# Kernel tuning notes

Hardware: AMD Instinct MI355X
Metric: run time of the kernel (lower is better)

The kernel has to match this reference:

```python
import jax, jax.numpy as jnp
import numpy as np

EPS = 1e-8
ACT_BITS = 8


def _ternary_vq(t):
    gamma = jnp.abs(t).mean()
    q = jnp.clip(jnp.round(t / (gamma + EPS)), -1.0, 1.0)
    return q * gamma


def setup_inputs() -> dict:
    key = jax.random.key(0)
    k1, k2, k3 = jax.random.split(key, 3)
    in_features, out_features = 1024, 1024
    x = jax.random.normal(k1, (8, 4096, in_features), dtype=jnp.float32)
    weight = jax.random.normal(k2, (out_features, in_features), dtype=jnp.float32)
    bias = jax.random.normal(k3, (out_features,), dtype=jnp.float32)
    return {"x": x, "weight": weight, "bias": bias}


def reference(x, weight, bias):
    # Weight/bias ternary quantization (done once in __init__ of the module)
    wq = _ternary_vq(weight)   # [out, in]
    bq = _ternary_vq(bias)     # [out]

    # Activation quantization: power-of-two scale from global absmax
    qmax = jnp.float32(2 ** (ACT_BITS - 1) - 1)  # 127
    max_val = jnp.max(jnp.abs(x))
    scale = jnp.exp2(jnp.floor(jnp.log2(max_val / qmax + EPS)))
    xq = jnp.round(jnp.clip(x, -qmax * scale, qmax * scale) / scale) * scale

    # F.linear: x @ W^T + b
    return jnp.einsum('bsi,oi->bso', xq, wq) + bq
```

## Files before the change

### kernel.cpp

```cpp
#include <hip/hip_runtime.h>

typedef __attribute__((ext_vector_type(4))) int int4v;

constexpr int Mdim = 32768;
constexpr int Kdim = 1024;
constexpr int Ndim = 1024;
constexpr float FEPS = 1e-8f;

constexpr size_t WQ_OFF = 32768;
constexpr size_t XQ_OFF = WQ_OFF + (size_t)Ndim * Kdim;
constexpr size_t WS_NEED = XQ_OFF + (size_t)Mdim * Kdim;

__device__ __forceinline__ void gload16(const void* g, void* l) {
  __builtin_amdgcn_global_load_lds(
      (const __attribute__((address_space(1))) unsigned int*)g,
      (__attribute__((address_space(3))) unsigned int*)l, 16, 0, 0);
}

__global__ void k_absmax(const uint4* __restrict__ xv, unsigned* __restrict__ pmax, int n4) {
  int i0 = blockIdx.x * blockDim.x + threadIdx.x;
  int stride = gridDim.x * blockDim.x;
  unsigned m = 0u;
  for (int i = i0; i < n4; i += stride) {
    uint4 v = xv[i];
    m = max(m, v.x & 0x7fffffffu);
    m = max(m, v.y & 0x7fffffffu);
    m = max(m, v.z & 0x7fffffffu);
    m = max(m, v.w & 0x7fffffffu);
  }
  #pragma unroll
  for (int off = 32; off > 0; off >>= 1)
    m = max(m, (unsigned)__shfl_down((int)m, off, 64));
  __shared__ unsigned red[4];
  if ((threadIdx.x & 63) == 0) red[threadIdx.x >> 6] = m;
  __syncthreads();
  if (threadIdx.x == 0) {
    unsigned r = max(max(red[0], red[1]), max(red[2], red[3]));
    pmax[blockIdx.x] = r;
  }
}

__global__ void k_wsum(const float4* __restrict__ wv, float* __restrict__ partials, int n4) {
  float s = 0.f;
  int stride = gridDim.x * blockDim.x;
  for (int i = blockIdx.x * blockDim.x + threadIdx.x; i < n4; i += stride) {
    float4 v = wv[i];
    s += fabsf(v.x) + fabsf(v.y) + fabsf(v.z) + fabsf(v.w);
  }
  __shared__ float red[256];
  red[threadIdx.x] = s;
  __syncthreads();
  for (int h = 128; h > 0; h >>= 1) {
    if (threadIdx.x < h) red[threadIdx.x] += red[threadIdx.x + h];
    __syncthreads();
  }
  if (threadIdx.x == 0) partials[blockIdx.x] = red[0];
}

__global__ void k_finalize(const float* __restrict__ bias, const float* __restrict__ partials,
                           const unsigned* __restrict__ pmax,
                           float* __restrict__ scalars, float* __restrict__ bq) {
  __shared__ float redf[256];
  __shared__ unsigned redu[256];
  __shared__ float sh_gb;
  int t = threadIdx.x;

  float s = fabsf(bias[t]) + fabsf(bias[t + 256]) + fabsf(bias[t + 512]) + fabsf(bias[t + 768]);
  redf[t] = s;
  unsigned m = 0u;
  #pragma unroll
  for (int i = 0; i < 8; ++i) m = max(m, pmax[t + 256 * i]);
  redu[t] = m;
  __syncthreads();
  for (int h = 128; h > 0; h >>= 1) {
    if (t < h) {
      redf[t] += redf[t + h];
      redu[t] = max(redu[t], redu[t + h]);
    }
    __syncthreads();
  }
  if (t == 0) {
    float gb = redf[0] / 1024.0f;
    float sw = 0.f;
    for (int i = 0; i < 256; ++i) sw += partials[i];
    float gw = sw / (1024.0f * 1024.0f);
    float maxval = __uint_as_float(redu[0]);
    float v = maxval / 127.0f + FEPS;
    int e = (int)((__float_as_uint(v) >> 23) & 0xff) - 127;
    float scale = ldexpf(1.0f, e);
    scalars[0] = gw;
    scalars[1] = gb;
    scalars[2] = scale;
    scalars[3] = scale * gw;
    scalars[4] = 127.0f * scale;
    scalars[5] = ldexpf(1.0f, -e);
    sh_gb = gb;
  }
  __syncthreads();
  float gb = sh_gb;
  for (int i = t; i < 1024; i += 256) {
    float q = rintf(bias[i] / (gb + FEPS));
    q = fminf(fmaxf(q, -1.0f), 1.0f);
    bq[i] = q * gb;
  }
}

__device__ __forceinline__ int qact8(float v, float qs, float inv) {
  return (int)rintf(fminf(fmaxf(v, -qs), qs) * inv);
}

__global__ void k_wquant(const float* __restrict__ w, const float* __restrict__ scalars,
                         unsigned char* __restrict__ wq) {
  float inv_g = scalars[0] + FEPS;
  int wave = (blockIdx.x * blockDim.x + threadIdx.x) >> 6;
  int lane = threadIdx.x & 63;
  int nb = wave >> 4;
  int kt = wave & 15;
  int r = lane >> 2;
  int c = lane & 3;
  const float4* src = (const float4*)(w + (size_t)(nb * 16 + r) * Kdim + kt * 64 + c * 16);
  unsigned o[4];
  #pragma unroll
  for (int v = 0; v < 4; ++v) {
    float4 f = src[v];
    int a = (int)rintf(fminf(fmaxf(f.x / inv_g, -1.f), 1.f));
    int b = (int)rintf(fminf(fmaxf(f.y / inv_g, -1.f), 1.f));
    int cc = (int)rintf(fminf(fmaxf(f.z / inv_g, -1.f), 1.f));
    int d = (int)rintf(fminf(fmaxf(f.w / inv_g, -1.f), 1.f));
    o[v] = (unsigned)(a & 0xff) | ((unsigned)(b & 0xff) << 8) |
           ((unsigned)(cc & 0xff) << 16) | ((unsigned)(d & 0xff) << 24);
  }
  uint4 pk; pk.x = o[0]; pk.y = o[1]; pk.z = o[2]; pk.w = o[3];
  *(uint4*)(wq + (size_t)wave * 1024 + c * 256 + r * 16) = pk;
}

__global__ void k_xquant(const float* __restrict__ x, const float* __restrict__ scalars,
                         unsigned char* __restrict__ xq) {
  float qs = scalars[4], inv = scalars[5];
  int wave = (blockIdx.x * blockDim.x + threadIdx.x) >> 6;
  int lane = threadIdx.x & 63;
  int mb = wave >> 4;
  int kt = wave & 15;
  int r = lane >> 2;
  int c = lane & 3;
  const float4* src = (const float4*)(x + (size_t)(mb * 16 + r) * Kdim + kt * 64 + c * 16);
  unsigned o[4];
  #pragma unroll
  for (int v = 0; v < 4; ++v) {
    float4 f = src[v];
    o[v] = (unsigned)(qact8(f.x, qs, inv) & 0xff) |
           ((unsigned)(qact8(f.y, qs, inv) & 0xff) << 8) |
           ((unsigned)(qact8(f.z, qs, inv) & 0xff) << 16) |
           ((unsigned)(qact8(f.w, qs, inv) & 0xff) << 24);
  }
  uint4 pk; pk.x = o[0]; pk.y = o[1]; pk.z = o[2]; pk.w = o[3];
  *(uint4*)(xq + (size_t)wave * 1024 + c * 256 + r * 16) = pk;
}

__launch_bounds__(256)
__global__ void k_gemm(const unsigned char* __restrict__ xq, const unsigned char* __restrict__ wq,
                       const float* __restrict__ scalars, const float* __restrict__ bq,
                       float* __restrict__ out) {
  __shared__ __align__(16) unsigned char lds[3 * 16384];

  const int tid = threadIdx.x;
  const int lane = tid & 63;
  const int wv = tid >> 6;
  const int wr = wv >> 1;
  const int wc = wv & 1;

  int bid = blockIdx.x;
  int swz = (bid & 7) * ((int)gridDim.x >> 3) + (bid >> 3);
  const int mtile = swz >> 3;
  const int ntile = swz & 7;
  const int m0 = mtile * 128;
  const int n0 = ntile * 128;

  const unsigned char* gA0 = xq + ((size_t)(mtile * 8 + wv) * 16) * 1024 + lane * 16;
  const unsigned char* gA1 = xq + ((size_t)(mtile * 8 + wv + 4) * 16) * 1024 + lane * 16;
  const unsigned char* gB0 = wq + ((size_t)(ntile * 8 + wv) * 16) * 1024 + lane * 16;
  const unsigned char* gB1 = wq + ((size_t)(ntile * 8 + wv + 4) * 16) * 1024 + lane * 16;
  const int lA0 = wv * 1024, lA1 = (wv + 4) * 1024;
  const int lB0 = 8192 + wv * 1024, lB1 = 8192 + (wv + 4) * 1024;

#define STAGE(kt, buf) do {                                   \
    unsigned char* base_ = lds + (buf) * 16384;               \
    gload16(gA0 + (size_t)(kt) * 1024, base_ + lA0);          \
    gload16(gA1 + (size_t)(kt) * 1024, base_ + lA1);          \
    gload16(gB0 + (size_t)(kt) * 1024, base_ + lB0);          \
    gload16(gB1 + (size_t)(kt) * 1024, base_ + lB1);          \
  } while (0)

  int4v acc[4][4];
  #pragma unroll
  for (int i = 0; i < 4; ++i)
    #pragma unroll
    for (int j = 0; j < 4; ++j)
      acc[i][j] = (int4v){0, 0, 0, 0};

  const int aoff = wr * 4 * 1024 + lane * 16;
  const int boff = 8192 + wc * 4 * 1024 + lane * 16;

  STAGE(0, 0);
  STAGE(1, 1);

  int cur = 0;
  for (int kt = 0; kt < 15; ++kt) {
    asm volatile("s_waitcnt vmcnt(4)" ::: "memory");
    __builtin_amdgcn_s_barrier();
    asm volatile("" ::: "memory");
    const unsigned char* bufp = lds + cur * 16384;
    int4v a[4], b[4];
    #pragma unroll
    for (int mi = 0; mi < 4; ++mi)
      a[mi] = *(const int4v*)(bufp + aoff + mi * 1024);
    #pragma unroll
    for (int ni = 0; ni < 4; ++ni)
      b[ni] = *(const int4v*)(bufp + boff + ni * 1024);
    if (kt < 14) {
      int nb = cur + 2; if (nb >= 3) nb -= 3;
      STAGE(kt + 2, nb);
    }
    #pragma unroll
    for (int mi = 0; mi < 4; ++mi)
      #pragma unroll
      for (int ni = 0; ni < 4; ++ni)
        acc[mi][ni] = __builtin_amdgcn_mfma_i32_16x16x64_i8(a[mi], b[ni], acc[mi][ni], 0, 0, 0);
    cur = (cur == 2) ? 0 : cur + 1;
  }
  asm volatile("s_waitcnt vmcnt(0)" ::: "memory");
  __builtin_amdgcn_s_barrier();
  asm volatile("" ::: "memory");
  {
    const unsigned char* bufp = lds + cur * 16384;
    int4v a[4], b[4];
    #pragma unroll
    for (int mi = 0; mi < 4; ++mi)
      a[mi] = *(const int4v*)(bufp + aoff + mi * 1024);
    #pragma unroll
    for (int ni = 0; ni < 4; ++ni)
      b[ni] = *(const int4v*)(bufp + boff + ni * 1024);
    #pragma unroll
    for (int mi = 0; mi < 4; ++mi)
      #pragma unroll
      for (int ni = 0; ni < 4; ++ni)
        acc[mi][ni] = __builtin_amdgcn_mfma_i32_16x16x64_i8(a[mi], b[ni], acc[mi][ni], 0, 0, 0);
  }
#undef STAGE

  const float sg = scalars[3];
  const int fr = lane & 15;
  #pragma unroll
  for (int ni = 0; ni < 4; ++ni) {
    const int col = n0 + wc * 64 + ni * 16 + fr;
    const float bb = bq[col];
    #pragma unroll
    for (int mi = 0; mi < 4; ++mi) {
      const int rowb = m0 + wr * 64 + mi * 16 + (lane >> 4) * 4;
      #pragma unroll
      for (int r = 0; r < 4; ++r)
        out[(size_t)(rowb + r) * Ndim + col] = (float)acc[mi][ni][r] * sg + bb;
    }
  }
}

extern "C" void kernel_launch(void* const* d_in, const int* in_sizes, int n_in,
                              void* d_out, int out_size, void* d_ws, size_t ws_size,
                              hipStream_t stream) {
  const float* x = (const float*)d_in[0];
  const float* weight = (const float*)d_in[1];
  const float* bias = (const float*)d_in[2];
  float* out = (float*)d_out;

  if (ws_size < WS_NEED) return;

  char* ws = (char*)d_ws;
  float* scalars = (float*)ws;
  float* partials = (float*)(ws + 1024);
  unsigned* pmax = (unsigned*)(ws + 4096);
  float* bq = (float*)(ws + 16384);
  unsigned char* wq = (unsigned char*)(ws + WQ_OFF);
  unsigned char* xq = (unsigned char*)(ws + XQ_OFF);

  k_absmax<<<2048, 256, 0, stream>>>((const uint4*)x, pmax, Mdim * Kdim / 4);
  k_wsum<<<256, 256, 0, stream>>>((const float4*)weight, partials, Ndim * Kdim / 4);
  k_finalize<<<1, 256, 0, stream>>>(bias, partials, pmax, scalars, bq);
  k_wquant<<<256, 256, 0, stream>>>(weight, scalars, wq);
  k_xquant<<<8192, 256, 0, stream>>>(x, scalars, xq);
  k_gemm<<<2048, 256, 0, stream>>>(xq, wq, scalars, bq, out);
}
```

Before: 112.2 us.

## Merge pre-pass and quantization kernels, change quant lane mapping, raise MFMA priority

Combines the absmax and weight-sum reductions into one launch, and the weight and activation quantization kernels into one launch, using block-index branching. This cuts the number of kernel launches and lets small kernels overlap with large ones. The quant lane mapping changes to r=lane&15, c=lane>>4 with a contiguous lane*16 store, so the write pattern differs while the packed layout should stay the same. The GEMM raises wave priority around the MFMA block with s_setprio to favour matrix issue over memory waves.

```diff
diff --git a/kernel.cpp b/kernel.cpp
--- a/kernel.cpp
+++ b/kernel.cpp
@@ -17,44 +17,47 @@
       (__attribute__((address_space(3))) unsigned int*)l, 16, 0, 0);
 }
 
-__global__ void k_absmax(const uint4* __restrict__ xv, unsigned* __restrict__ pmax, int n4) {
-  int i0 = blockIdx.x * blockDim.x + threadIdx.x;
-  int stride = gridDim.x * blockDim.x;
-  unsigned m = 0u;
-  for (int i = i0; i < n4; i += stride) {
-    uint4 v = xv[i];
-    m = max(m, v.x & 0x7fffffffu);
-    m = max(m, v.y & 0x7fffffffu);
-    m = max(m, v.z & 0x7fffffffu);
-    m = max(m, v.w & 0x7fffffffu);
-  }
-  #pragma unroll
-  for (int off = 32; off > 0; off >>= 1)
-    m = max(m, (unsigned)__shfl_down((int)m, off, 64));
-  __shared__ unsigned red[4];
-  if ((threadIdx.x & 63) == 0) red[threadIdx.x >> 6] = m;
-  __syncthreads();
-  if (threadIdx.x == 0) {
-    unsigned r = max(max(red[0], red[1]), max(red[2], red[3]));
-    pmax[blockIdx.x] = r;
-  }
-}
-
-__global__ void k_wsum(const float4* __restrict__ wv, float* __restrict__ partials, int n4) {
-  float s = 0.f;
-  int stride = gridDim.x * blockDim.x;
-  for (int i = blockIdx.x * blockDim.x + threadIdx.x; i < n4; i += stride) {
-    float4 v = wv[i];
-    s += fabsf(v.x) + fabsf(v.y) + fabsf(v.z) + fabsf(v.w);
-  }
-  __shared__ float red[256];
-  red[threadIdx.x] = s;
-  __syncthreads();
-  for (int h = 128; h > 0; h >>= 1) {
-    if (threadIdx.x < h) red[threadIdx.x] += red[threadIdx.x + h];
+__global__ void k_pre(const uint4* __restrict__ xv, const float4* __restrict__ wv,
+                      unsigned* __restrict__ pmax, float* __restrict__ partials) {
+  const int tid = threadIdx.x;
+  if (blockIdx.x < 2048) {
+    int i0 = blockIdx.x * 256 + tid;
+    const int stride = 2048 * 256;
+    const int n4 = Mdim * Kdim / 4;
+    unsigned m = 0u;
+    for (int i = i0; i < n4; i += stride) {
+      uint4 v = xv[i];
+      m = max(m, v.x & 0x7fffffffu);
+      m = max(m, v.y & 0x7fffffffu);
+      m = max(m, v.z & 0x7fffffffu);
+      m = max(m, v.w & 0x7fffffffu);
+    }
+    #pragma unroll
+    for (int off = 32; off > 0; off >>= 1)
+      m = max(m, (unsigned)__shfl_down((int)m, off, 64));
+    __shared__ unsigned red[4];
+    if ((tid & 63) == 0) red[tid >> 6] = m;
     __syncthreads();
-  }
-  if (threadIdx.x == 0) partials[blockIdx.x] = red[0];
+    if (tid == 0)
+      pmax[blockIdx.x] = max(max(red[0], red[1]), max(red[2], red[3]));
+  } else {
+    int wb = blockIdx.x - 2048;
+    float s = 0.f;
+    const int stride = 256 * 256;
+    const int n4 = Ndim * Kdim / 4;
+    for (int i = wb * 256 + tid; i < n4; i += stride) {
+      float4 v = wv[i];
+      s += fabsf(v.x) + fabsf(v.y) + fabsf(v.z) + fabsf(v.w);
+    }
+    __shared__ float red[256];
+    red[tid] = s;
+    __syncthreads();
+    for (int h = 128; h > 0; h >>= 1) {
+      if (tid < h) red[tid] += red[tid + h];
+      __syncthreads();
+    }
+    if (tid == 0) partials[wb] = red[0];
+  }
 }
 
 __global__ void k_finalize(const float* __restrict__ bias, const float* __restrict__ partials,
@@ -109,52 +112,50 @@
   return (int)rintf(fminf(fmaxf(v, -qs), qs) * inv);
 }
 
-__global__ void k_wquant(const float* __restrict__ w, const float* __restrict__ scalars,
-                         unsigned char* __restrict__ wq) {
-  float inv_g = scalars[0] + FEPS;
-  int wave = (blockIdx.x * blockDim.x + threadIdx.x) >> 6;
-  int lane = threadIdx.x & 63;
-  int nb = wave >> 4;
-  int kt = wave & 15;
-  int r = lane >> 2;
-  int c = lane & 3;
-  const float4* src = (const float4*)(w + (size_t)(nb * 16 + r) * Kdim + kt * 64 + c * 16);
-  unsigned o[4];
-  #pragma unroll
-  for (int v = 0; v < 4; ++v) {
-    float4 f = src[v];
-    int a = (int)rintf(fminf(fmaxf(f.x / inv_g, -1.f), 1.f));
-    int b = (int)rintf(fminf(fmaxf(f.y / inv_g, -1.f), 1.f));
-    int cc = (int)rintf(fminf(fmaxf(f.z / inv_g, -1.f), 1.f));
-    int d = (int)rintf(fminf(fmaxf(f.w / inv_g, -1.f), 1.f));
-    o[v] = (unsigned)(a & 0xff) | ((unsigned)(b & 0xff) << 8) |
-           ((unsigned)(cc & 0xff) << 16) | ((unsigned)(d & 0xff) << 24);
-  }
-  uint4 pk; pk.x = o[0]; pk.y = o[1]; pk.z = o[2]; pk.w = o[3];
-  *(uint4*)(wq + (size_t)wave * 1024 + c * 256 + r * 16) = pk;
-}
-
-__global__ void k_xquant(const float* __restrict__ x, const float* __restrict__ scalars,
-                         unsigned char* __restrict__ xq) {
-  float qs = scalars[4], inv = scalars[5];
-  int wave = (blockIdx.x * blockDim.x + threadIdx.x) >> 6;
-  int lane = threadIdx.x & 63;
-  int mb = wave >> 4;
-  int kt = wave & 15;
-  int r = lane >> 2;
-  int c = lane & 3;
-  const float4* src = (const float4*)(x + (size_t)(mb * 16 + r) * Kdim + kt * 64 + c * 16);
-  unsigned o[4];
-  #pragma unroll
-  for (int v = 0; v < 4; ++v) {
-    float4 f = src[v];
-    o[v] = (unsigned)(qact8(f.x, qs, inv) & 0xff) |
-           ((unsigned)(qact8(f.y, qs, inv) & 0xff) << 8) |
-           ((unsigned)(qact8(f.z, qs, inv) & 0xff) << 16) |
-           ((unsigned)(qact8(f.w, qs, inv) & 0xff) << 24);
-  }
-  uint4 pk; pk.x = o[0]; pk.y = o[1]; pk.z = o[2]; pk.w = o[3];
-  *(uint4*)(xq + (size_t)wave * 1024 + c * 256 + r * 16) = pk;
+__global__ void k_quant(const float* __restrict__ x, const float* __restrict__ w,
+                        const float* __restrict__ scalars,
+                        unsigned char* __restrict__ xq, unsigned char* __restrict__ wq) {
+  const int tid = threadIdx.x;
+  const int lane = tid & 63;
+  const int r = lane & 15;
+  const int c = lane >> 4;
+  if (blockIdx.x < 8192) {
+    float qs = scalars[4], inv = scalars[5];
+    int wave = blockIdx.x * 4 + (tid >> 6);
+    int mb = wave >> 4;
+    int kt = wave & 15;
+    const float4* src = (const float4*)(x + (size_t)(mb * 16 + r) * Kdim + kt * 64 + c * 16);
+    unsigned o[4];
+    #pragma unroll
+    for (int v = 0; v < 4; ++v) {
+      float4 f = src[v];
+      o[v] = (unsigned)(qact8(f.x, qs, inv) & 0xff) |
+             ((unsigned)(qact8(f.y, qs, inv) & 0xff) << 8) |
+             ((unsigned)(qact8(f.z, qs, inv) & 0xff) << 16) |
+             ((unsigned)(qact8(f.w, qs, inv) & 0xff) << 24);
+    }
+    uint4 pk; pk.x = o[0]; pk.y = o[1]; pk.z = o[2]; pk.w = o[3];
+    *(uint4*)(xq + (size_t)wave * 1024 + lane * 16) = pk;
+  } else {
+    float inv_g = scalars[0] + FEPS;
+    int wave = (blockIdx.x - 8192) * 4 + (tid >> 6);
+    int nb = wave >> 4;
+    int kt = wave & 15;
+    const float4* src = (const float4*)(w + (size_t)(nb * 16 + r) * Kdim + kt * 64 + c * 16);
+    unsigned o[4];
+    #pragma unroll
+    for (int v = 0; v < 4; ++v) {
+      float4 f = src[v];
+      int a = (int)rintf(fminf(fmaxf(f.x / inv_g, -1.f), 1.f));
+      int b = (int)rintf(fminf(fmaxf(f.y / inv_g, -1.f), 1.f));
+      int cc = (int)rintf(fminf(fmaxf(f.z / inv_g, -1.f), 1.f));
+      int d = (int)rintf(fminf(fmaxf(f.w / inv_g, -1.f), 1.f));
+      o[v] = (unsigned)(a & 0xff) | ((unsigned)(b & 0xff) << 8) |
+             ((unsigned)(cc & 0xff) << 16) | ((unsigned)(d & 0xff) << 24);
+    }
+    uint4 pk; pk.x = o[0]; pk.y = o[1]; pk.z = o[2]; pk.w = o[3];
+    *(uint4*)(wq + (size_t)wave * 1024 + lane * 16) = pk;
+  }
 }
 
 __launch_bounds__(256)
@@ -221,11 +222,13 @@
       int nb = cur + 2; if (nb >= 3) nb -= 3;
       STAGE(kt + 2, nb);
     }
+    __builtin_amdgcn_s_setprio(1);
     #pragma unroll
     for (int mi = 0; mi < 4; ++mi)
       #pragma unroll
       for (int ni = 0; ni < 4; ++ni)
         acc[mi][ni] = __builtin_amdgcn_mfma_i32_16x16x64_i8(a[mi], b[ni], acc[mi][ni], 0, 0, 0);
+    __builtin_amdgcn_s_setprio(0);
     cur = (cur == 2) ? 0 : cur + 1;
   }
   asm volatile("s_waitcnt vmcnt(0)" ::: "memory");
@@ -240,11 +243,13 @@
     #pragma unroll
     for (int ni = 0; ni < 4; ++ni)
       b[ni] = *(const int4v*)(bufp + boff + ni * 1024);
+    __builtin_amdgcn_s_setprio(1);
     #pragma unroll
     for (int mi = 0; mi < 4; ++mi)
       #pragma unroll
       for (int ni = 0; ni < 4; ++ni)
         acc[mi][ni] = __builtin_amdgcn_mfma_i32_16x16x64_i8(a[mi], b[ni], acc[mi][ni], 0, 0, 0);
+    __builtin_amdgcn_s_setprio(0);
   }
 #undef STAGE
 
@@ -282,10 +287,8 @@
   unsigned char* wq = (unsigned char*)(ws + WQ_OFF);
   unsigned char* xq = (unsigned char*)(ws + XQ_OFF);
 
-  k_absmax<<<2048, 256, 0, stream>>>((const uint4*)x, pmax, Mdim * Kdim / 4);
-  k_wsum<<<256, 256, 0, stream>>>((const float4*)weight, partials, Ndim * Kdim / 4);
+  k_pre<<<2304, 256, 0, stream>>>((const uint4*)x, (const float4*)weight, pmax, partials);
   k_finalize<<<1, 256, 0, stream>>>(bias, partials, pmax, scalars, bq);
-  k_wquant<<<256, 256, 0, stream>>>(weight, scalars, wq);
-  k_xquant<<<8192, 256, 0, stream>>>(x, scalars, xq);
+  k_quant<<<8448, 256, 0, stream>>>(x, weight, scalars, xq, wq);
   k_gemm<<<2048, 256, 0, stream>>>(xq, wq, scalars, bq, out);
 }
```

After: 103.1 us. 8.1% less time.
